# Kernel optimization log

Hardware: AMD Instinct MI355X
Metric: run time of the kernel (lower is better)

Reference implementation:

```python
import jax, jax.numpy as jnp
import numpy as np

B = 4096    # batch
IN = 2048   # input_dim of mapper
N = 512     # n: dim of linear subspace (z)
K = 1024    # k: ambient dim (y)
NQ = 8      # number of quadratic constraints
M_ROWS = 2 * N  # linear inequality rows (box)


def setup_inputs() -> dict:
    key = jax.random.key(0)
    ks = jax.random.split(key, 6)
    x = jax.random.normal(ks[0], (B, IN), jnp.float32)
    # mapper: Linear(IN -> N+1)
    W_map = jax.random.normal(ks[1], (N + 1, IN), jnp.float32) / np.float32(np.sqrt(IN))
    b_map = jnp.zeros((N + 1,), jnp.float32)
    # Linear constraints in the subspace: box |z_j| <= 1, with z0 = 0 strictly feasible
    eye_n = jnp.eye(N, dtype=jnp.float32)
    A_p = jnp.concatenate([eye_n, -eye_n], axis=0)          # [2N, N]
    b_p = jnp.ones((M_ROWS, 1), jnp.float32)
    z0 = jnp.zeros((N, 1), jnp.float32)
    # D = A_p / ((b_p - A_p @ z0) @ ones(1,N))  -- row-wise slack normalization
    D = A_p / (b_p - A_p @ z0)                              # [2N, N]
    # Affine lift y = NA_E @ z + y1
    NA_E = jax.random.normal(ks[2], (K, N), jnp.float32) / np.float32(np.sqrt(N))
    y1 = 0.01 * jax.random.normal(ks[3], (K, 1), jnp.float32)
    # Quadratic constraints 0.5 y^T P y + q^T y + r <= 0, P PSD (>= 2I)
    Mrand = jax.random.normal(ks[4], (NQ, K, K), jnp.float32)
    all_P = 2.0 * (jnp.einsum('ikm,ijm->ikj', Mrand, Mrand) / K + jnp.eye(K, dtype=jnp.float32))
    all_q = jnp.zeros((NQ, K, 1), jnp.float32)
    # choose r so that y0 = NA_E@z0 + y1 is strictly interior: c = -1
    w = (NA_E @ z0 + y1)[:, 0]                              # [K]
    half_wPw = 0.5 * jnp.einsum('k,ikj,j->i', w, all_P, w)  # [NQ]
    all_r = (-(half_wPw + all_q[:, :, 0] @ w) - 1.0).reshape(NQ, 1, 1)
    return dict(x=x, W_map=W_map, b_map=b_map, D=D, NA_E=NA_E, y1=y1, z0=z0,
                all_P=all_P, all_q=all_q, all_r=all_r)


def _forward(x, W_map, b_map, D, NA_E, y1, z0, all_P, all_q, all_r):
    # mapper: input -> [B, N+1]
    qm = x @ W_map.T + b_map
    v = qm[:, :N]                                   # direction in subspace [B, N]
    beta = qm[:, N]                                 # scalar per sample [B]
    # v_bar = normalize(v) (torch F.normalize semantics, eps=1e-12)
    vn = jnp.linalg.norm(v, axis=1, keepdims=True)
    v_bar = v / jnp.maximum(vn, 1e-12)
    # kappa from linear constraints: relu(max_j (D @ v_bar)_j)
    kappa = jax.nn.relu(jnp.max(v_bar @ D.T, axis=1))        # [B]
    # kappa from quadratic constraints
    w = (NA_E @ z0 + y1)[:, 0]                      # y0 in ambient space [K]
    rho = v_bar @ NA_E.T                            # [B, K]
    Prho = jnp.einsum('ikj,bj->bik', all_P, rho)    # [B, NQ, K]
    a = 0.5 * jnp.einsum('bik,bk->bi', Prho, rho)   # [B, NQ]
    Pw_plus_q = jnp.einsum('ikj,j->ik', all_P, w) + all_q[:, :, 0]  # [NQ, K]
    bq = rho @ Pw_plus_q.T                          # [B, NQ]
    c = 0.5 * jnp.einsum('k,ikj,j->i', w, all_P, w) + all_q[:, :, 0] @ w + all_r[:, 0, 0]  # [NQ]
    disc = bq * bq - 4.0 * a * c                    # > 0 since c < 0, a > 0
    lam = (-bq + jnp.sqrt(disc)) / (2.0 * a)        # max step along v_bar per constraint
    kappa = jnp.maximum(kappa, jnp.max(1.0 / lam, axis=1))
    # walker_2: alpha = 1 / (exp(beta) + kappa)  (<= 1/kappa, guaranteed feasible)
    alpha = 1.0 / (jnp.exp(beta) + kappa)           # [B]
    z = z0[:, 0] + alpha[:, None] * v_bar           # [B, N]
    y = z @ NA_E.T + y1[:, 0]                       # getyFromz: y = NA_E z + y1, [B, K]
    return y


def reference(x, W_map, b_map, D, NA_E, y1, z0, all_P, all_q, all_r):
    return _forward(x, W_map, b_map, D, NA_E, y1, z0, all_P, all_q, all_r)
```

## Files before the change

### kernel.cpp

```cpp
#include <hip/hip_runtime.h>

#define B_ROWS 4096
#define IN_DIM 2048
#define N_DIM  512
#define K_DIM  1024
#define NQ     8

typedef __attribute__((ext_vector_type(8))) short short8;
typedef __attribute__((ext_vector_type(8))) unsigned short ushort8;
typedef __attribute__((ext_vector_type(4))) float f32x4;

constexpr size_t OFF_REGA  = 0;
constexpr size_t OFF_REGB  = 16777216;
constexpr size_t OFF_GBF   = 25165824;
constexpr size_t OFF_NAEBF = 29360128;
constexpr size_t OFF_NAETB = 30408704;
constexpr size_t OFF_WVBF  = 31457280;
constexpr size_t OFF_QMV   = 33554432;
constexpr size_t OFF_VBARB = 41943040;
constexpr size_t OFF_BETA  = 46137344;
constexpr size_t OFF_KAP   = OFF_BETA + 16384;
constexpr size_t OFF_W     = OFF_KAP  + 16384;
constexpr size_t OFF_PWQ   = OFF_W    + 4096;
constexpr size_t OFF_C     = OFF_PWQ  + 32768;
constexpr size_t OFF_ASUM  = OFF_C    + 1024;

__device__ __forceinline__ unsigned short f2bf(float f) {
    unsigned int u = __builtin_bit_cast(unsigned int, f);
    u = (u + 0x7fffu + ((u >> 16) & 1u)) >> 16;
    return (unsigned short)u;
}
__device__ __forceinline__ float bf2f(unsigned short h) {
    unsigned int u = ((unsigned int)h) << 16;
    return __builtin_bit_cast(float, u);
}
__device__ __forceinline__ void gll16(const void* g, void* l) {
    __builtin_amdgcn_global_load_lds(
        (const __attribute__((address_space(1))) unsigned int*)g,
        (__attribute__((address_space(3))) unsigned int*)l, 16, 0, 0);
}

template<int BM, int BN, int MODE>
__global__ __launch_bounds__(256)
void mfma_abt(const unsigned short* __restrict__ A,
              const unsigned short* __restrict__ Bm,
              float* __restrict__ Cf, unsigned short* __restrict__ Cb,
              int N, int Kd, int lda, int ldb,
              const float* __restrict__ bias,
              const unsigned short* __restrict__ red, int ishift,
              float* __restrict__ aout,
              long sA, long sB, long sC)
{
    constexpr int FM = BM / 32, FN = BN / 32;
    __shared__ unsigned short As[BM * 32];
    __shared__ unsigned short Bs[BN * 32];
    A  += (size_t)sA * blockIdx.z;
    Bm += (size_t)sB * blockIdx.z;
    const int tid  = threadIdx.x;
    const int lane = tid & 63, wave = tid >> 6;
    const int wm = wave >> 1, wn = wave & 1;
    const int lg = lane >> 4, lr = lane & 15;
    const int m0 = blockIdx.y * BM, n0 = blockIdx.x * BN;

    f32x4 acc[FM][FN] = {};

    for (int k0 = 0; k0 < Kd; k0 += 32) {
        #pragma unroll
        for (int r = 0; r < BM / 64; ++r) {
            const int l16 = (r << 8) + tid;
            const int row = l16 >> 2;
            const int c8  = (l16 & 3) << 3;
            gll16(&A[(size_t)(m0 + row) * lda + k0 + c8], &As[(size_t)l16 << 3]);
        }
        #pragma unroll
        for (int r = 0; r < BN / 64; ++r) {
            const int l16 = (r << 8) + tid;
            const int row = l16 >> 2;
            const int c8  = (l16 & 3) << 3;
            gll16(&Bm[(size_t)(n0 + row) * ldb + k0 + c8], &Bs[(size_t)l16 << 3]);
        }
        __syncthreads();
        short8 af[FM], bfr[FN];
        #pragma unroll
        for (int f = 0; f < FM; ++f)
            af[f]  = *reinterpret_cast<const short8*>(&As[(wm * (BM/2) + f * 16 + lr) * 32 + lg * 8]);
        #pragma unroll
        for (int f = 0; f < FN; ++f)
            bfr[f] = *reinterpret_cast<const short8*>(&Bs[(wn * (BN/2) + f * 16 + lr) * 32 + lg * 8]);
        #pragma unroll
        for (int fm = 0; fm < FM; ++fm)
            #pragma unroll
            for (int fn = 0; fn < FN; ++fn)
                acc[fm][fn] = __builtin_amdgcn_mfma_f32_16x16x32_bf16(
                                  af[fm], bfr[fn], acc[fm][fn], 0, 0, 0);
        __syncthreads();
    }

    if constexpr (MODE == 0) {
        #pragma unroll
        for (int fm = 0; fm < FM; ++fm)
            #pragma unroll
            for (int r = 0; r < 4; ++r) {
                const int m = m0 + wm * (BM/2) + fm * 16 + lg * 4 + r;
                #pragma unroll
                for (int fn = 0; fn < FN; ++fn) {
                    const int n = n0 + wn * (BN/2) + fn * 16 + lr;
                    Cf[(size_t)m * N + n] = acc[fm][fn][r] + (bias ? bias[n] : 0.f);
                }
            }
    } else if constexpr (MODE == 1) {
        unsigned short* C = Cb + (size_t)sC * blockIdx.z;
        #pragma unroll
        for (int fm = 0; fm < FM; ++fm)
            #pragma unroll
            for (int r = 0; r < 4; ++r) {
                const int m = m0 + wm * (BM/2) + fm * 16 + lg * 4 + r;
                #pragma unroll
                for (int fn = 0; fn < FN; ++fn) {
                    const int n = n0 + wn * (BN/2) + fn * 16 + lr;
                    C[(size_t)m * N + n] = f2bf(acc[fm][fn][r]);
                }
            }
    } else {
        const int i = n0 >> ishift;
        const int mask = (1 << ishift) - 1;
        #pragma unroll
        for (int fm = 0; fm < FM; ++fm)
            #pragma unroll
            for (int r = 0; r < 4; ++r) {
                const int m = m0 + wm * (BM/2) + fm * 16 + lg * 4 + r;
                float p = 0.f;
                #pragma unroll
                for (int fn = 0; fn < FN; ++fn) {
                    const int ng = (n0 & mask) + wn * (BN/2) + fn * 16 + lr;
                    p = fmaf(acc[fm][fn][r], bf2f(red[(size_t)m * (mask + 1) + ng]), p);
                }
                #pragma unroll
                for (int off = 1; off < 16; off <<= 1) p += __shfl_xor(p, off);
                if (lr == 0) atomicAdd(&aout[(size_t)m * NQ + i], p);
            }
    }
}

__global__ __launch_bounds__(256)
void kprep(const float* __restrict__ all_P, const float* __restrict__ W_map,
           const float* __restrict__ NA_E, const float* __restrict__ z0,
           const float* __restrict__ y1,
           unsigned short* __restrict__ P_bf, unsigned short* __restrict__ Wv_bf,
           unsigned short* __restrict__ nae_bf, unsigned short* __restrict__ naet_bf,
           float* __restrict__ w)
{
    int id = blockIdx.x;
    const int tid = threadIdx.x;
    const float* src = nullptr; unsigned short* dst = nullptr;
    if (id < 4096)       { src = all_P; dst = P_bf; }
    else if (id < 4608)  { id -= 4096; src = W_map; dst = Wv_bf; }
    else if (id < 4864)  { id -= 4608; src = NA_E;  dst = nae_bf; }
    if (src) {
        const size_t base = ((size_t)id * 2048) + (size_t)tid * 8;
        const float4 a = *reinterpret_cast<const float4*>(&src[base]);
        const float4 b = *reinterpret_cast<const float4*>(&src[base + 4]);
        ushort8 o;
        o[0] = f2bf(a.x); o[1] = f2bf(a.y); o[2] = f2bf(a.z); o[3] = f2bf(a.w);
        o[4] = f2bf(b.x); o[5] = f2bf(b.y); o[6] = f2bf(b.z); o[7] = f2bf(b.w);
        *reinterpret_cast<ushort8*>(&dst[base]) = o;
        return;
    }
    if (id < 5376) {
        id -= 4864;
        const int bx = id & 15, by = id >> 4;
        __shared__ float t[32][33];
        const int r = tid & 31, c = tid >> 5;
        #pragma unroll
        for (int cc = c; cc < 32; cc += 8)
            t[cc][r] = NA_E[(size_t)(by * 32 + cc) * N_DIM + bx * 32 + r];
        __syncthreads();
        #pragma unroll
        for (int cc = c; cc < 32; cc += 8)
            naet_bf[(size_t)(bx * 32 + cc) * K_DIM + by * 32 + r] = f2bf(t[r][cc]);
        return;
    }
    {
        const int k = id - 5376;
        const float* rw = NA_E + (size_t)k * N_DIM;
        float s = fmaf(rw[tid], z0[tid], rw[tid + 256] * z0[tid + 256]);
        #pragma unroll
        for (int off = 32; off; off >>= 1) s += __shfl_down(s, off);
        __shared__ float red[4];
        if ((tid & 63) == 0) red[tid >> 6] = s;
        __syncthreads();
        if (tid == 0) w[k] = red[0] + red[1] + red[2] + red[3] + y1[k];
    }
}

__global__ __launch_bounds__(256)
void kbetax(const float* __restrict__ x, const float* __restrict__ W_map,
            const float* __restrict__ b_map, float* __restrict__ beta,
            unsigned short* __restrict__ x_bf)
{
    const int b = blockIdx.x, tid = threadIdx.x;
    const float* xr = x + (size_t)b * IN_DIM;
    const float* wr = W_map + (size_t)N_DIM * IN_DIM;
    const float4 xa = *reinterpret_cast<const float4*>(&xr[tid * 8]);
    const float4 xb = *reinterpret_cast<const float4*>(&xr[tid * 8 + 4]);
    const float4 wa = *reinterpret_cast<const float4*>(&wr[tid * 8]);
    const float4 wb = *reinterpret_cast<const float4*>(&wr[tid * 8 + 4]);
    ushort8 o;
    o[0] = f2bf(xa.x); o[1] = f2bf(xa.y); o[2] = f2bf(xa.z); o[3] = f2bf(xa.w);
    o[4] = f2bf(xb.x); o[5] = f2bf(xb.y); o[6] = f2bf(xb.z); o[7] = f2bf(xb.w);
    *reinterpret_cast<ushort8*>(&x_bf[(size_t)b * IN_DIM + tid * 8]) = o;
    float s = xa.x * wa.x + xa.y * wa.y + xa.z * wa.z + xa.w * wa.w
            + xb.x * wb.x + xb.y * wb.y + xb.z * wb.z + xb.w * wb.w;
    #pragma unroll
    for (int off = 32; off; off >>= 1) s += __shfl_down(s, off);
    __shared__ float red[4];
    if ((tid & 63) == 0) red[tid >> 6] = s;
    __syncthreads();
    if (tid == 0) beta[b] = red[0] + red[1] + red[2] + red[3] + b_map[N_DIM];
}

__global__ __launch_bounds__(256)
void knorm(const float* __restrict__ qm, unsigned short* __restrict__ vbarbf,
           float* __restrict__ kap0)
{
    const int b = blockIdx.x, tid = threadIdx.x;
    const float v0 = qm[(size_t)b * N_DIM + tid];
    const float v1 = qm[(size_t)b * N_DIM + tid + 256];
    float s = fmaf(v0, v0, v1 * v1);
    #pragma unroll
    for (int off = 32; off; off >>= 1) s += __shfl_down(s, off);
    __shared__ float rs[4]; __shared__ float sden;
    if ((tid & 63) == 0) rs[tid >> 6] = s;
    __syncthreads();
    if (tid == 0) sden = fmaxf(sqrtf(rs[0] + rs[1] + rs[2] + rs[3]), 1e-12f);
    __syncthreads();
    const float b0 = v0 / sden, b1 = v1 / sden;
    vbarbf[(size_t)b * N_DIM + tid]       = f2bf(b0);
    vbarbf[(size_t)b * N_DIM + tid + 256] = f2bf(b1);
    float m = fmaxf(fabsf(b0), fabsf(b1));
    #pragma unroll
    for (int off = 32; off; off >>= 1) m = fmaxf(m, __shfl_down(m, off));
    __shared__ float rm[4];
    if ((tid & 63) == 0) rm[tid >> 6] = m;
    __syncthreads();
    if (tid == 0) kap0[b] = fmaxf(fmaxf(rm[0], rm[1]), fmaxf(rm[2], rm[3]));
}

__global__ __launch_bounds__(256)
void kpwq(const float* __restrict__ P, const float* __restrict__ q,
          const float* __restrict__ w, float* __restrict__ Pwq)
{
    const int row = blockIdx.x, tid = threadIdx.x;
    const float* Pr = P + ((size_t)row << 10);
    float s = 0.f;
    #pragma unroll
    for (int t = 0; t < 4; ++t) {
        const int j = tid + 256 * t;
        s = fmaf(Pr[j], w[j], s);
    }
    #pragma unroll
    for (int off = 32; off; off >>= 1) s += __shfl_down(s, off);
    __shared__ float red[4];
    if ((tid & 63) == 0) red[tid >> 6] = s;
    __syncthreads();
    if (tid == 0) Pwq[row] = red[0] + red[1] + red[2] + red[3] + q[row];
}

__global__ __launch_bounds__(256)
void kc(const float* __restrict__ Pwq, const float* __restrict__ q,
        const float* __restrict__ w, const float* __restrict__ rr,
        float* __restrict__ c)
{
    const int i = blockIdx.x, tid = threadIdx.x;
    float s = 0.f;
    for (int k = tid; k < K_DIM; k += 256) {
        const float wk = w[k];
        s = fmaf(wk, Pwq[i * K_DIM + k], s);
        s = fmaf(q[i * K_DIM + k], wk, s);
    }
    #pragma unroll
    for (int off = 32; off; off >>= 1) s += __shfl_down(s, off);
    __shared__ float red[4];
    if ((tid & 63) == 0) red[tid >> 6] = s;
    __syncthreads();
    if (tid == 0) c[i] = 0.5f * (red[0] + red[1] + red[2] + red[3]) + rr[i];
}

__global__ __launch_bounds__(256)
void kfinal(const float* __restrict__ rho, const float* __restrict__ asum,
            const float* __restrict__ Pwq, const float* __restrict__ c,
            const float* __restrict__ kap0, const float* __restrict__ beta,
            const float* __restrict__ w, float* __restrict__ y)
{
    const int b = blockIdx.x, tid = threadIdx.x;
    __shared__ float rsh[K_DIM];
    const float* rrow = rho + (size_t)b * K_DIM;
    #pragma unroll
    for (int t = 0; t < 4; ++t) rsh[tid + 256 * t] = rrow[tid + 256 * t];
    __syncthreads();

    __shared__ float bqsh[NQ];
    const int i = tid >> 5, lane32 = tid & 31;
    float s = 0.f;
    for (int k = lane32; k < K_DIM; k += 32)
        s = fmaf(rsh[k], Pwq[i * K_DIM + k], s);
    #pragma unroll
    for (int off = 16; off; off >>= 1) s += __shfl_xor(s, off);
    if (lane32 == 0) bqsh[i] = s;
    __syncthreads();

    __shared__ float salpha;
    if (tid == 0) {
        float kap = kap0[b];
        float invmax = -3.4e38f;
        #pragma unroll
        for (int q_ = 0; q_ < NQ; ++q_) {
            const float a    = 0.5f * asum[(size_t)b * NQ + q_];
            const float bqv  = bqsh[q_];
            const float disc = bqv * bqv - 4.f * a * c[q_];
            const float lam  = (-bqv + sqrtf(disc)) / (2.f * a);
            invmax = fmaxf(invmax, 1.f / lam);
        }
        kap = fmaxf(kap, invmax);
        salpha = 1.f / (expf(beta[b]) + kap);
    }
    __syncthreads();
    const float alpha = salpha;
    #pragma unroll
    for (int t = 0; t < 4; ++t) {
        const int k = tid + 256 * t;
        y[(size_t)b * K_DIM + k] = fmaf(alpha, rsh[k], w[k]);
    }
}

extern "C" void kernel_launch(void* const* d_in, const int* in_sizes, int n_in,
                              void* d_out, int out_size, void* d_ws, size_t ws_size,
                              hipStream_t stream)
{
    const float* x     = (const float*)d_in[0];
    const float* W_map = (const float*)d_in[1];
    const float* b_map = (const float*)d_in[2];
    const float* NA_E  = (const float*)d_in[4];
    const float* y1    = (const float*)d_in[5];
    const float* z0    = (const float*)d_in[6];
    const float* all_P = (const float*)d_in[7];
    const float* all_q = (const float*)d_in[8];
    const float* all_r = (const float*)d_in[9];
    float* y = (float*)d_out;

    char* ws = (char*)d_ws;
    unsigned short* P_bf    = (unsigned short*)(ws + OFF_REGA);
    unsigned short* x_bf    = (unsigned short*)(ws + OFF_REGA);
    float*          rho     = (float*)         (ws + OFF_REGA);
    unsigned short* Tt_bf   = (unsigned short*)(ws + OFF_REGB);
    unsigned short* G_bf    = (unsigned short*)(ws + OFF_GBF);
    unsigned short* nae_bf  = (unsigned short*)(ws + OFF_NAEBF);
    unsigned short* naet_bf = (unsigned short*)(ws + OFF_NAETB);
    unsigned short* Wv_bf   = (unsigned short*)(ws + OFF_WVBF);
    float*          qm_v    = (float*)(ws + OFF_QMV);
    unsigned short* vbar_bf = (unsigned short*)(ws + OFF_VBARB);
    float* beta = (float*)(ws + OFF_BETA);
    float* kap0 = (float*)(ws + OFF_KAP);
    float* w    = (float*)(ws + OFF_W);
    float* Pwq  = (float*)(ws + OFF_PWQ);
    float* c    = (float*)(ws + OFF_C);
    float* asum = (float*)(ws + OFF_ASUM);

    hipMemsetAsync(asum, 0, (size_t)B_ROWS * NQ * sizeof(float), stream);

    kprep<<<6400, 256, 0, stream>>>(all_P, W_map, NA_E, z0, y1,
                                    P_bf, Wv_bf, nae_bf, naet_bf, w);
    kpwq<<<NQ * K_DIM, 256, 0, stream>>>(all_P, all_q, w, Pwq);
    kc  <<<NQ, 256, 0, stream>>>(Pwq, all_q, w, all_r, c);

    mfma_abt<64, 64, 1><<<dim3(16, 8, 8), 256, 0, stream>>>(
        naet_bf, P_bf, nullptr, Tt_bf, 1024, 1024, 1024, 1024,
        nullptr, nullptr, 0, nullptr, 0, (long)K_DIM * K_DIM, (long)N_DIM * K_DIM);
    mfma_abt<64, 64, 1><<<dim3(8, 8, 8), 256, 0, stream>>>(
        naet_bf, Tt_bf, nullptr, G_bf, 512, 1024, 1024, 1024,
        nullptr, nullptr, 0, nullptr, 0, (long)N_DIM * K_DIM, (long)N_DIM * N_DIM);

    kbetax<<<B_ROWS, 256, 0, stream>>>(x, W_map, b_map, beta, x_bf);

    mfma_abt<64, 64, 0><<<dim3(8, 64), 256, 0, stream>>>(
        x_bf, Wv_bf, qm_v, nullptr, 512, 2048, 2048, 2048,
        b_map, nullptr, 0, nullptr, 0, 0, 0);
    knorm<<<B_ROWS, 256, 0, stream>>>(qm_v, vbar_bf, kap0);

    mfma_abt<64, 64, 0><<<dim3(16, 64), 256, 0, stream>>>(
        vbar_bf, nae_bf, rho, nullptr, 1024, 512, 512, 512,
        nullptr, nullptr, 0, nullptr, 0, 0, 0);

    mfma_abt<128, 128, 2><<<dim3(32, 32), 256, 0, stream>>>(
        vbar_bf, G_bf, nullptr, nullptr, 4096, 512, 512, 512,
        nullptr, vbar_bf, 9, asum, 0, 0, 0);

    kfinal<<<B_ROWS, 256, 0, stream>>>(rho, asum, Pwq, c, kap0, beta, w, y);
}
```

Baseline: 295.1 us.

## Double-buffer LDS tiles and exploit P symmetry to halve quadratic-form GEMM work

```diff
diff --git a/kernel.cpp b/kernel.cpp
--- a/kernel.cpp
+++ b/kernel.cpp
@@ -52,8 +52,8 @@
               long sA, long sB, long sC)
 {
     constexpr int FM = BM / 32, FN = BN / 32;
-    __shared__ unsigned short As[BM * 32];
-    __shared__ unsigned short Bs[BN * 32];
+    __shared__ unsigned short As[2][BM * 32];
+    __shared__ unsigned short Bs[2][BN * 32];
     A  += (size_t)sA * blockIdx.z;
     Bm += (size_t)sB * blockIdx.z;
     const int tid  = threadIdx.x;
@@ -62,31 +62,58 @@
     const int lg = lane >> 4, lr = lane & 15;
     const int m0 = blockIdx.y * BM, n0 = blockIdx.x * BN;
 
+    const int mask = (1 << ishift) - 1;
+    int nt, diagStep;
+    if constexpr (MODE == 2) {
+        nt = ((n0 & mask) + BN) >> 5;
+        diagStep = (n0 & mask) >> 5;
+    } else {
+        nt = Kd >> 5; diagStep = -1;
+    }
+
     f32x4 acc[FM][FN] = {};
 
-    for (int k0 = 0; k0 < Kd; k0 += 32) {
+    auto STAGE = [&](int buf, int k0) {
         #pragma unroll
         for (int r = 0; r < BM / 64; ++r) {
             const int l16 = (r << 8) + tid;
             const int row = l16 >> 2;
             const int c8  = (l16 & 3) << 3;
-            gll16(&A[(size_t)(m0 + row) * lda + k0 + c8], &As[(size_t)l16 << 3]);
+            gll16(&A[(size_t)(m0 + row) * lda + k0 + c8], &As[buf][(size_t)l16 << 3]);
         }
         #pragma unroll
         for (int r = 0; r < BN / 64; ++r) {
             const int l16 = (r << 8) + tid;
             const int row = l16 >> 2;
             const int c8  = (l16 & 3) << 3;
-            gll16(&Bm[(size_t)(n0 + row) * ldb + k0 + c8], &Bs[(size_t)l16 << 3]);
+            gll16(&Bm[(size_t)(n0 + row) * ldb + k0 + c8], &Bs[buf][(size_t)l16 << 3]);
         }
-        __syncthreads();
+    };
+
+    STAGE(0, 0);
+    __syncthreads();
+    int cur = 0;
+
+    for (int t = 0; t < nt; ++t) {
+        if (t + 1 < nt) STAGE(cur ^ 1, (t + 1) << 5);
+        if constexpr (MODE == 2) {
+            if (t == diagStep) {
+                #pragma unroll
+                for (int fm = 0; fm < FM; ++fm)
+                    #pragma unroll
+                    for (int fn = 0; fn < FN; ++fn)
+                        #pragma unroll
+                        for (int r = 0; r < 4; ++r)
+                            acc[fm][fn][r] *= 2.0f;
+            }
+        }
         short8 af[FM], bfr[FN];
         #pragma unroll
         for (int f = 0; f < FM; ++f)
-            af[f]  = *reinterpret_cast<const short8*>(&As[(wm * (BM/2) + f * 16 + lr) * 32 + lg * 8]);
+            af[f]  = *reinterpret_cast<const short8*>(&As[cur][(wm * (BM/2) + f * 16 + lr) * 32 + lg * 8]);
         #pragma unroll
         for (int f = 0; f < FN; ++f)
-            bfr[f] = *reinterpret_cast<const short8*>(&Bs[(wn * (BN/2) + f * 16 + lr) * 32 + lg * 8]);
+            bfr[f] = *reinterpret_cast<const short8*>(&Bs[cur][(wn * (BN/2) + f * 16 + lr) * 32 + lg * 8]);
         #pragma unroll
         for (int fm = 0; fm < FM; ++fm)
             #pragma unroll
@@ -94,6 +121,7 @@
                 acc[fm][fn] = __builtin_amdgcn_mfma_f32_16x16x32_bf16(
                                   af[fm], bfr[fn], acc[fm][fn], 0, 0, 0);
         __syncthreads();
+        cur ^= 1;
     }
 
     if constexpr (MODE == 0) {
@@ -123,7 +151,6 @@
             }
     } else {
         const int i = n0 >> ishift;
-        const int mask = (1 << ishift) - 1;
         #pragma unroll
         for (int fm = 0; fm < FM; ++fm)
             #pragma unroll
```

Result: faster. 283.4 us (-4.0%).
